# Kernel optimization log

Measured on AMD Instinct MI355X. Metric: run time of the kernel, lower is better.

The kernel has to match this reference:

```python
import jax, jax.numpy as jnp
import numpy as np

B, T, C = 2, 2048, 768
H = 12
D = C // H
HID = 4 * C
EPS = 1e-5
LS_INIT = 1e-4


def _ln(x, g, b):
    mu = jnp.mean(x, axis=-1, keepdims=True)
    var = jnp.mean((x - mu) ** 2, axis=-1, keepdims=True)
    return (x - mu) * jax.lax.rsqrt(var + EPS) * g + b


def setup_inputs() -> dict:
    key = jax.random.key(0)
    ks = jax.random.split(key, 10)
    s = lambda fan_in: 1.0 / np.sqrt(fan_in)
    return {
        "x": jax.random.normal(ks[0], (B, T, C), dtype=jnp.float32),
        "mask_logits": jnp.zeros((B, 1, T, T), dtype=jnp.float32),
        "bias": jax.random.normal(ks[1], (B, H, T, T), dtype=jnp.float32),
        "ln1_g": jnp.ones((C,), jnp.float32),
        "ln1_b": jnp.zeros((C,), jnp.float32),
        "qkv_w": jax.random.normal(ks[2], (3 * C, C), jnp.float32) * s(C),
        "qkv_b": jnp.zeros((3 * C,), jnp.float32),
        "proj_w": jax.random.normal(ks[3], (C, C), jnp.float32) * s(C),
        "proj_b": jnp.zeros((C,), jnp.float32),
        "ls1": jnp.full((C,), LS_INIT, jnp.float32),
        "ln2_g": jnp.ones((C,), jnp.float32),
        "ln2_b": jnp.zeros((C,), jnp.float32),
        "w1": jax.random.normal(ks[4], (HID, C), jnp.float32) * s(C),
        "b1": jnp.zeros((HID,), jnp.float32),
        "w2": jax.random.normal(ks[5], (C, HID), jnp.float32) * s(HID),
        "b2": jnp.zeros((C,), jnp.float32),
        "ls2": jnp.full((C,), LS_INIT, jnp.float32),
    }


def reference(x, mask_logits, bias, ln1_g, ln1_b, qkv_w, qkv_b, proj_w, proj_b,
              ls1, ln2_g, ln2_b, w1, b1, w2, b2, ls2):
    scale = 1.0 / np.sqrt(D)
    xn = _ln(x, ln1_g, ln1_b)
    qkv = xn @ qkv_w.T + qkv_b                      # [B,T,3C]
    qkv = qkv.reshape(B, T, 3, H, D).transpose(2, 0, 3, 1, 4)  # [3,B,H,T,D]
    q, k, v = qkv[0], qkv[1], qkv[2]
    logits = jnp.einsum('bhqd,bhkd->bhqk', q, k) * scale + bias + mask_logits
    attn = jax.nn.softmax(logits, axis=-1)          # [B,H,T,T]
    y = jnp.einsum('bhqk,bhkd->bhqd', attn, v)      # [B,H,T,D]
    y = y.transpose(0, 2, 1, 3).reshape(B, T, C)
    y = y @ proj_w.T + proj_b
    x = x + y * ls1
    h = _ln(x, ln2_g, ln2_b)
    h = jax.nn.gelu(h @ w1.T + b1, approximate=False)
    h = h @ w2.T + b2
    x = x + h * ls2
    return x, jax.lax.stop_gradient(attn)
```

## Files before the change

### kernel.cpp

```cpp
#include <hip/hip_runtime.h>
#include <hip/hip_bf16.h>
#include <math.h>

#define B_ 2
#define T_ 2048
#define C_ 768
#define H_ 12
#define D_ 64
#define HID_ 3072
#define NROW 4096
#define N3C 2304

typedef short bf16x8 __attribute__((ext_vector_type(8)));
typedef float f32x4 __attribute__((ext_vector_type(4)));
typedef unsigned short u16;
typedef unsigned int u32;

__device__ inline u16 f2bf(float f) {
    u32 u = __float_as_uint(f);
    u32 r = (u + 0x7fffu + ((u >> 16) & 1u)) >> 16;
    return (u16)r;
}

__global__ __launch_bounds__(256) void cvt_bf16_kernel(const float* __restrict__ s,
                                                       u16* __restrict__ d, int n) {
    int i = (blockIdx.x * 256 + threadIdx.x) * 4;
    if (i >= n) return;
    float4 v = *(const float4*)(s + i);
    ushort4 o;
    o.x = f2bf(v.x); o.y = f2bf(v.y); o.z = f2bf(v.z); o.w = f2bf(v.w);
    *(ushort4*)(d + i) = o;
}

__global__ __launch_bounds__(256) void ln_kernel(const float* __restrict__ x,
                                                 const float* __restrict__ g,
                                                 const float* __restrict__ b,
                                                 u16* __restrict__ out) {
    int row = blockIdx.x, t = threadIdx.x;
    const float* xr = x + (size_t)row * C_;
    float v[3], s = 0.f, sq = 0.f;
#pragma unroll
    for (int i = 0; i < 3; i++) {
        v[i] = xr[i * 256 + t];
        s += v[i]; sq += v[i] * v[i];
    }
    for (int m = 32; m; m >>= 1) { s += __shfl_xor(s, m); sq += __shfl_xor(sq, m); }
    __shared__ float ss[4], ssq[4];
    int wid = t >> 6;
    if ((t & 63) == 0) { ss[wid] = s; ssq[wid] = sq; }
    __syncthreads();
    s = ss[0] + ss[1] + ss[2] + ss[3];
    sq = ssq[0] + ssq[1] + ssq[2] + ssq[3];
    float mu = s * (1.f / C_);
    float var = sq * (1.f / C_) - mu * mu;
    float rstd = rsqrtf(var + 1e-5f);
#pragma unroll
    for (int i = 0; i < 3; i++) {
        int c = i * 256 + t;
        out[(size_t)row * C_ + c] = f2bf((v[i] - mu) * rstd * g[c] + b[c]);
    }
}

template <int EPI>
__global__ __launch_bounds__(256) void gemm_kernel(const u16* __restrict__ A,
                                                   const u16* __restrict__ W,
                                                   const float* __restrict__ bias,
                                                   float* __restrict__ outf,
                                                   u16* __restrict__ outb,
                                                   const float* __restrict__ res,
                                                   const float* __restrict__ ls,
                                                   int N, int K) {
    __shared__ u16 Alds[128 * 64];
    __shared__ u16 Blds[128 * 64];
    int tid = threadIdx.x;
    int m0 = blockIdx.y * 128, n0 = blockIdx.x * 128;
    int lane = tid & 63, wid = tid >> 6;
    int wr = wid >> 1, wc = wid & 1;
    int lr = lane & 15, lq = lane >> 4;

    f32x4 acc[4][4];
#pragma unroll
    for (int i = 0; i < 4; i++)
#pragma unroll
        for (int j = 0; j < 4; j++) acc[i][j] = (f32x4){0.f, 0.f, 0.f, 0.f};

    int nk = K >> 6;
    const u16* Ab = A + (size_t)m0 * K;
    const u16* Wb = W + (size_t)n0 * K;
    bf16x8 ra[4], rb[4];
#pragma unroll
    for (int i = 0; i < 4; i++) {
        int c = tid + i * 256, row = c >> 3, j = c & 7;
        ra[i] = *(const bf16x8*)(Ab + (size_t)row * K + j * 8);
        rb[i] = *(const bf16x8*)(Wb + (size_t)row * K + j * 8);
    }
    for (int kt = 0; kt < nk; ++kt) {
        __syncthreads();
#pragma unroll
        for (int i = 0; i < 4; i++) {
            int c = tid + i * 256, row = c >> 3, j = c & 7;
            int off = row * 64 + ((j ^ (row & 7)) << 3);
            *(bf16x8*)(Alds + off) = ra[i];
            *(bf16x8*)(Blds + off) = rb[i];
        }
        __syncthreads();
        if (kt + 1 < nk) {
            int k0 = (kt + 1) << 6;
#pragma unroll
            for (int i = 0; i < 4; i++) {
                int c = tid + i * 256, row = c >> 3, j = c & 7;
                ra[i] = *(const bf16x8*)(Ab + (size_t)row * K + k0 + j * 8);
                rb[i] = *(const bf16x8*)(Wb + (size_t)row * K + k0 + j * 8);
            }
        }
#pragma unroll
        for (int s = 0; s < 2; s++) {
            bf16x8 af[4], bw[4];
#pragma unroll
            for (int i = 0; i < 4; i++) {
                int arow = wr * 64 + i * 16 + lr;
                af[i] = *(const bf16x8*)(Alds + arow * 64 + (((4 * s + lq) ^ (arow & 7)) << 3));
                int brow = wc * 64 + i * 16 + lr;
                bw[i] = *(const bf16x8*)(Blds + brow * 64 + (((4 * s + lq) ^ (brow & 7)) << 3));
            }
#pragma unroll
            for (int i = 0; i < 4; i++)
#pragma unroll
                for (int j = 0; j < 4; j++)
                    acc[i][j] = __builtin_amdgcn_mfma_f32_16x16x32_bf16(af[i], bw[j], acc[i][j], 0, 0, 0);
        }
    }
#pragma unroll
    for (int i = 0; i < 4; i++) {
#pragma unroll
        for (int j = 0; j < 4; j++) {
#pragma unroll
            for (int r = 0; r < 4; r++) {
                int gm = m0 + wr * 64 + i * 16 + lq * 4 + r;
                int gn = n0 + wc * 64 + j * 16 + lr;
                float val = acc[i][j][r] + bias[gn];
                if (EPI == 0) {
                    outb[(size_t)gm * N + gn] = f2bf(val);
                } else if (EPI == 1) {
                    float gl = 0.5f * val * (1.f + erff(val * 0.70710678118654752f));
                    outb[(size_t)gm * N + gn] = f2bf(gl);
                } else {
                    outf[(size_t)gm * N + gn] = res[(size_t)gm * N + gn] + ls[gn] * val;
                }
            }
        }
    }
}

__global__ __launch_bounds__(256) void vtrans_kernel(const u16* __restrict__ qkv,
                                                     u16* __restrict__ vt) {
    __shared__ u16 tile[64 * 72];
    int t0 = blockIdx.x * 64, h = blockIdx.y, b = blockIdx.z;
    int tid = threadIdx.x;
#pragma unroll
    for (int i = 0; i < 2; i++) {
        int c = tid + i * 256, tr = c >> 3, j = c & 7;
        bf16x8 v = *(const bf16x8*)(qkv + (size_t)(b * T_ + t0 + tr) * N3C + 1536 + h * 64 + j * 8);
        *(bf16x8*)(tile + tr * 72 + j * 8) = v;
    }
    __syncthreads();
#pragma unroll
    for (int i = 0; i < 2; i++) {
        int c = tid + i * 256, d = c >> 3, tj = c & 7;
        bf16x8 o;
#pragma unroll
        for (int k = 0; k < 8; k++) o[k] = (short)tile[(tj * 8 + k) * 72 + d];
        *(bf16x8*)(vt + (size_t)((b * H_ + h) * 64 + d) * T_ + t0 + tj * 8) = o;
    }
}

__global__ __launch_bounds__(256, 2) void attn_kernel(const u16* __restrict__ qkv,
                                                      const u16* __restrict__ vt,
                                                      const float* __restrict__ bias,
                                                      const float* __restrict__ mask,
                                                      float* __restrict__ attn_out,
                                                      u16* __restrict__ ybuf) {
    __shared__ u16 S[16 * 2048];
    __shared__ float rinv_lds[16];
    char* Sb = (char*)S;
    int qt = blockIdx.x, h = blockIdx.y, b = blockIdx.z;
    int tid = threadIdx.x, lane = tid & 63, wid = tid >> 6;
    int lr = lane & 15, lq = lane >> 4;
    int q0 = qt * 16;
    size_t bh = (size_t)(b * H_ + h);
    const float scale = 0.125f;

    const u16* qp = qkv + (size_t)(b * T_ + q0 + lr) * N3C + h * 64;
    bf16x8 qa0 = *(const bf16x8*)(qp + lq * 8);
    bf16x8 qa1 = *(const bf16x8*)(qp + 32 + lq * 8);
    const float* bp = bias + (bh * T_ + q0 + lr) * T_;
    const float* mp = mask + ((size_t)b * T_ + q0 + lr) * T_;
#pragma unroll 4
    for (int ct = 0; ct < 32; ++ct) {
        int colbase = wid * 512 + ct * 16;
        const u16* kp = qkv + (size_t)(b * T_ + colbase + lr) * N3C + 768 + h * 64;
        bf16x8 kf0 = *(const bf16x8*)(kp + lq * 8);
        bf16x8 kf1 = *(const bf16x8*)(kp + 32 + lq * 8);
        float4 b4 = *(const float4*)(bp + colbase + lq * 4);
        float4 m4 = *(const float4*)(mp + colbase + lq * 4);
        f32x4 a = (f32x4){0.f, 0.f, 0.f, 0.f};
        a = __builtin_amdgcn_mfma_f32_16x16x32_bf16(kf0, qa0, a, 0, 0, 0);
        a = __builtin_amdgcn_mfma_f32_16x16x32_bf16(kf1, qa1, a, 0, 0, 0);
        ushort4 pk;
        pk.x = f2bf(a[0] * scale + b4.x + m4.x);
        pk.y = f2bf(a[1] * scale + b4.y + m4.y);
        pk.z = f2bf(a[2] * scale + b4.z + m4.z);
        pk.w = f2bf(a[3] * scale + b4.w + m4.w);
        *(ushort4*)(Sb + (((u32)lr * 4096 + 2 * colbase + 8 * lq) ^ ((lr & 7) << 4))) = pk;
    }
    __syncthreads();

    float* ao_base = attn_out + (bh * T_ + q0) * T_;
#pragma unroll 1
    for (int rr = 0; rr < 4; ++rr) {
        int r = wid * 4 + rr;
        u32 rowb = (u32)r * 4096;
        int swz = (r & 7) << 4;
        u32 pk[16];
        float mx = -1e30f;
#pragma unroll
        for (int i = 0; i < 16; i++) {
            pk[i] = *(u32*)(Sb + ((rowb + i * 256 + 4 * lane) ^ swz));
            float lo = __uint_as_float(pk[i] << 16);
            float hi = __uint_as_float(pk[i] & 0xffff0000u);
            mx = fmaxf(mx, fmaxf(lo, hi));
        }
        for (int m = 32; m; m >>= 1) mx = fmaxf(mx, __shfl_xor(mx, m));
        float e[32];
        float lsum = 0.f;
#pragma unroll
        for (int i = 0; i < 16; i++) {
            float lo = __uint_as_float(pk[i] << 16);
            float hi = __uint_as_float(pk[i] & 0xffff0000u);
            float e0 = __expf(lo - mx), e1 = __expf(hi - mx);
            e[2 * i] = e0; e[2 * i + 1] = e1;
            lsum += e0 + e1;
            u32 po = ((u32)f2bf(e1) << 16) | (u32)f2bf(e0);
            *(u32*)(Sb + ((rowb + i * 256 + 4 * lane) ^ swz)) = po;
        }
        for (int m = 32; m; m >>= 1) lsum += __shfl_xor(lsum, m);
        float rinv = 1.f / lsum;
        if (lane == 0) rinv_lds[r] = rinv;
        float* ao = ao_base + (size_t)r * T_;
#pragma unroll
        for (int i = 0; i < 16; i++) {
            float2 o;
            o.x = e[2 * i] * rinv;
            o.y = e[2 * i + 1] * rinv;
            *(float2*)(ao + i * 128 + 2 * lane) = o;
        }
    }
    __syncthreads();

    f32x4 acc = (f32x4){0.f, 0.f, 0.f, 0.f};
    const u16* vtp = vt + (bh * 64 + wid * 16 + lr) * (size_t)T_;
#pragma unroll 4
    for (int ks = 0; ks < 64; ++ks) {
        bf16x8 pf = *(const bf16x8*)(Sb + (((u32)lr * 4096 + ks * 64 + lq * 16) ^ ((lr & 7) << 4)));
        bf16x8 vf = *(const bf16x8*)(vtp + ks * 32 + lq * 8);
        acc = __builtin_amdgcn_mfma_f32_16x16x32_bf16(pf, vf, acc, 0, 0, 0);
    }
#pragma unroll
    for (int r = 0; r < 4; r++) {
        int row = lq * 4 + r;
        float y = acc[r] * rinv_lds[row];
        ybuf[(size_t)(b * T_ + q0 + row) * C_ + h * 64 + wid * 16 + lr] = f2bf(y);
    }
}

extern "C" void kernel_launch(void* const* d_in, const int* in_sizes, int n_in,
                              void* d_out, int out_size, void* d_ws, size_t ws_size,
                              hipStream_t stream) {
    const float* x = (const float*)d_in[0];
    const float* mask = (const float*)d_in[1];
    const float* bias = (const float*)d_in[2];
    const float* ln1g = (const float*)d_in[3];
    const float* ln1b = (const float*)d_in[4];
    const float* qkvw = (const float*)d_in[5];
    const float* qkvb = (const float*)d_in[6];
    const float* projw = (const float*)d_in[7];
    const float* projb = (const float*)d_in[8];
    const float* ls1 = (const float*)d_in[9];
    const float* ln2g = (const float*)d_in[10];
    const float* ln2b = (const float*)d_in[11];
    const float* w1 = (const float*)d_in[12];
    const float* b1 = (const float*)d_in[13];
    const float* w2 = (const float*)d_in[14];
    const float* b2 = (const float*)d_in[15];
    const float* ls2 = (const float*)d_in[16];

    char* ws = (char*)d_ws;
    size_t off = 0;
    u16* qkvw_b = (u16*)(ws + off); off += (size_t)N3C * C_ * 2;
    u16* projw_b = (u16*)(ws + off); off += (size_t)C_ * C_ * 2;
    u16* w1_b = (u16*)(ws + off); off += (size_t)HID_ * C_ * 2;
    u16* w2_b = (u16*)(ws + off); off += (size_t)C_ * HID_ * 2;
    u16* xn = (u16*)(ws + off); off += (size_t)NROW * C_ * 2;
    u16* qkvbuf = (u16*)(ws + off); off += (size_t)NROW * N3C * 2;
    u16* vt = (u16*)(ws + off); off += (size_t)B_ * H_ * D_ * T_ * 2;
    u16* g = qkvbuf;
    u16* ybuf = (u16*)(ws + off); off += (size_t)NROW * C_ * 2;
    float* x1 = (float*)(ws + off); off += (size_t)NROW * C_ * 4;
    (void)ws_size; (void)n_in; (void)in_sizes; (void)out_size;

    float* outx = (float*)d_out;
    float* attn_out = outx + (size_t)NROW * C_;

    cvt_bf16_kernel<<<(N3C * C_ / 4 + 255) / 256, 256, 0, stream>>>(qkvw, qkvw_b, N3C * C_);
    cvt_bf16_kernel<<<(C_ * C_ / 4 + 255) / 256, 256, 0, stream>>>(projw, projw_b, C_ * C_);
    cvt_bf16_kernel<<<(HID_ * C_ / 4 + 255) / 256, 256, 0, stream>>>(w1, w1_b, HID_ * C_);
    cvt_bf16_kernel<<<(C_ * HID_ / 4 + 255) / 256, 256, 0, stream>>>(w2, w2_b, C_ * HID_);

    ln_kernel<<<NROW, 256, 0, stream>>>(x, ln1g, ln1b, xn);
    gemm_kernel<0><<<dim3(N3C / 128, NROW / 128), 256, 0, stream>>>(
        xn, qkvw_b, qkvb, nullptr, qkvbuf, nullptr, nullptr, N3C, C_);
    vtrans_kernel<<<dim3(T_ / 64, H_, B_), 256, 0, stream>>>(qkvbuf, vt);
    attn_kernel<<<dim3(T_ / 16, H_, B_), 256, 0, stream>>>(qkvbuf, vt, bias, mask, attn_out, ybuf);
    gemm_kernel<2><<<dim3(C_ / 128, NROW / 128), 256, 0, stream>>>(
        ybuf, projw_b, projb, x1, nullptr, x, ls1, C_, C_);
    ln_kernel<<<NROW, 256, 0, stream>>>(x1, ln2g, ln2b, xn);
    gemm_kernel<1><<<dim3(HID_ / 128, NROW / 128), 256, 0, stream>>>(
        xn, w1_b, b1, nullptr, g, nullptr, nullptr, HID_, C_);
    gemm_kernel<2><<<dim3(C_ / 128, NROW / 128), 256, 0, stream>>>(
        g, w2_b, b2, outx, nullptr, x1, ls2, C_, HID_);
}
```

Before: 519.9 us.

## Split fused attention into QK-exp and PV kernels via global P buffer

Replaces the single LDS-heavy attention kernel with two kernels when the workspace is large enough. qk_kernel computes exp(logits) directly, without subtracting the row max, writes unnormalised bf16 probabilities to a global buffer and reduces the row sums. pv_kernel reads them back to write the normalised attention output and to compute P·V. The aim is to drop the 64KB LDS tile and its barriers so more blocks fit per CU. The cost is a large extra global round trip for P, and skipping the max subtraction risks overflow when logits are large.

```diff
diff --git a/kernel.cpp b/kernel.cpp
--- a/kernel.cpp
+++ b/kernel.cpp
@@ -174,6 +174,101 @@
     }
 }
 
+__global__ __launch_bounds__(256, 4) void qk_kernel(const u16* __restrict__ qkv,
+                                                    const float* __restrict__ bias,
+                                                    const float* __restrict__ mask,
+                                                    u16* __restrict__ p,
+                                                    float* __restrict__ lsum) {
+    __shared__ float red[4][16];
+    int qt = blockIdx.x, h = blockIdx.y, b = blockIdx.z;
+    int tid = threadIdx.x, lane = tid & 63, wid = tid >> 6;
+    int lr = lane & 15, lq = lane >> 4;
+    int q0 = qt * 16;
+    size_t bh = (size_t)(b * H_ + h);
+    const float scale = 0.125f;
+
+    const u16* qp = qkv + (size_t)(b * T_ + q0 + lr) * N3C + h * 64;
+    bf16x8 qa0 = *(const bf16x8*)(qp + lq * 8);
+    bf16x8 qa1 = *(const bf16x8*)(qp + 32 + lq * 8);
+    const float* bp = bias + (bh * T_ + q0 + lr) * T_ + wid * 512 + lq * 4;
+    const float* mp = mask + ((size_t)b * T_ + q0 + lr) * T_ + wid * 512 + lq * 4;
+    const u16* kbase = qkv + (size_t)(b * T_ + wid * 512 + lr) * N3C + 768 + h * 64 + lq * 8;
+    u16* pt = p + ((bh * 128 + qt) << 15) + (size_t)lr * 2048 + wid * 512 + lq * 4;
+
+    float ls = 0.f;
+#pragma unroll
+    for (int ct = 0; ct < 32; ++ct) {
+        bf16x8 kf0 = *(const bf16x8*)(kbase + (size_t)ct * 16 * N3C);
+        bf16x8 kf1 = *(const bf16x8*)(kbase + (size_t)ct * 16 * N3C + 32);
+        float4 b4 = *(const float4*)(bp + ct * 16);
+        float4 m4 = *(const float4*)(mp + ct * 16);
+        f32x4 a = (f32x4){0.f, 0.f, 0.f, 0.f};
+        a = __builtin_amdgcn_mfma_f32_16x16x32_bf16(kf0, qa0, a, 0, 0, 0);
+        a = __builtin_amdgcn_mfma_f32_16x16x32_bf16(kf1, qa1, a, 0, 0, 0);
+        float e0 = __expf(a[0] * scale + b4.x + m4.x);
+        float e1 = __expf(a[1] * scale + b4.y + m4.y);
+        float e2 = __expf(a[2] * scale + b4.z + m4.z);
+        float e3 = __expf(a[3] * scale + b4.w + m4.w);
+        ls += (e0 + e1) + (e2 + e3);
+        ushort4 pk;
+        pk.x = f2bf(e0); pk.y = f2bf(e1); pk.z = f2bf(e2); pk.w = f2bf(e3);
+        *(ushort4*)(pt + ct * 16) = pk;
+    }
+    ls += __shfl_xor(ls, 16);
+    ls += __shfl_xor(ls, 32);
+    if (lane < 16) red[wid][lr] = ls;
+    __syncthreads();
+    if (tid < 16)
+        lsum[bh * T_ + q0 + tid] = (red[0][tid] + red[1][tid]) + (red[2][tid] + red[3][tid]);
+}
+
+__global__ __launch_bounds__(256, 4) void pv_kernel(const u16* __restrict__ p,
+                                                    const u16* __restrict__ vt,
+                                                    const float* __restrict__ lsum,
+                                                    float* __restrict__ attn_out,
+                                                    u16* __restrict__ ybuf) {
+    int qt = blockIdx.x, h = blockIdx.y, b = blockIdx.z;
+    int tid = threadIdx.x, lane = tid & 63, wid = tid >> 6;
+    int lr = lane & 15, lq = lane >> 4;
+    int q0 = qt * 16;
+    size_t bh = (size_t)(b * H_ + h);
+    const u16* pt = p + ((bh * 128 + qt) << 15);
+    const float* lsb = lsum + bh * T_ + q0;
+
+    float* ao_base = attn_out + (bh * T_ + q0) * T_;
+#pragma unroll
+    for (int rr = 0; rr < 4; ++rr) {
+        int r = wid * 4 + rr;
+        float rinv = 1.f / lsb[r];
+        const u16* pr = pt + (size_t)r * 2048;
+        float* ao = ao_base + (size_t)r * T_;
+#pragma unroll
+        for (int i = 0; i < 16; i++) {
+            u32 pk2 = *(const u32*)(pr + i * 128 + 2 * lane);
+            float2 o;
+            o.x = __uint_as_float(pk2 << 16) * rinv;
+            o.y = __uint_as_float(pk2 & 0xffff0000u) * rinv;
+            *(float2*)(ao + i * 128 + 2 * lane) = o;
+        }
+    }
+
+    f32x4 acc = (f32x4){0.f, 0.f, 0.f, 0.f};
+    const u16* vtp = vt + (bh * 64 + wid * 16 + lr) * (size_t)T_ + lq * 8;
+    const u16* pr = pt + (size_t)lr * 2048 + lq * 8;
+#pragma unroll 8
+    for (int ks = 0; ks < 64; ++ks) {
+        bf16x8 pf = *(const bf16x8*)(pr + ks * 32);
+        bf16x8 vf = *(const bf16x8*)(vtp + ks * 32);
+        acc = __builtin_amdgcn_mfma_f32_16x16x32_bf16(pf, vf, acc, 0, 0, 0);
+    }
+#pragma unroll
+    for (int r = 0; r < 4; r++) {
+        int row = lq * 4 + r;
+        float y = acc[r] / lsb[row];
+        ybuf[(size_t)(b * T_ + q0 + row) * C_ + h * 64 + wid * 16 + lr] = f2bf(y);
+    }
+}
+
 __global__ __launch_bounds__(256, 2) void attn_kernel(const u16* __restrict__ qkv,
                                                       const u16* __restrict__ vt,
                                                       const float* __restrict__ bias,
@@ -193,19 +288,19 @@
     const u16* qp = qkv + (size_t)(b * T_ + q0 + lr) * N3C + h * 64;
     bf16x8 qa0 = *(const bf16x8*)(qp + lq * 8);
     bf16x8 qa1 = *(const bf16x8*)(qp + 32 + lq * 8);
-    const float* bp = bias + (bh * T_ + q0 + lr) * T_;
-    const float* mp = mask + ((size_t)b * T_ + q0 + lr) * T_;
+    const float* bp = bias + (bh * T_ + q0 + lr) * T_ + wid * 512 + lq * 4;
+    const float* mp = mask + ((size_t)b * T_ + q0 + lr) * T_ + wid * 512 + lq * 4;
+    const u16* kbase = qkv + (size_t)(b * T_ + wid * 512 + lr) * N3C + 768 + h * 64 + lq * 8;
 #pragma unroll 4
     for (int ct = 0; ct < 32; ++ct) {
-        int colbase = wid * 512 + ct * 16;
-        const u16* kp = qkv + (size_t)(b * T_ + colbase + lr) * N3C + 768 + h * 64;
-        bf16x8 kf0 = *(const bf16x8*)(kp + lq * 8);
-        bf16x8 kf1 = *(const bf16x8*)(kp + 32 + lq * 8);
-        float4 b4 = *(const float4*)(bp + colbase + lq * 4);
-        float4 m4 = *(const float4*)(mp + colbase + lq * 4);
+        bf16x8 kf0 = *(const bf16x8*)(kbase + (size_t)ct * 16 * N3C);
+        bf16x8 kf1 = *(const bf16x8*)(kbase + (size_t)ct * 16 * N3C + 32);
+        float4 b4 = *(const float4*)(bp + ct * 16);
+        float4 m4 = *(const float4*)(mp + ct * 16);
         f32x4 a = (f32x4){0.f, 0.f, 0.f, 0.f};
         a = __builtin_amdgcn_mfma_f32_16x16x32_bf16(kf0, qa0, a, 0, 0, 0);
         a = __builtin_amdgcn_mfma_f32_16x16x32_bf16(kf1, qa1, a, 0, 0, 0);
+        int colbase = wid * 512 + ct * 16;
         ushort4 pk;
         pk.x = f2bf(a[0] * scale + b4.x + m4.x);
         pk.y = f2bf(a[1] * scale + b4.y + m4.y);
@@ -232,19 +327,19 @@
         }
         for (int m = 32; m; m >>= 1) mx = fmaxf(mx, __shfl_xor(mx, m));
         float e[32];
-        float lsum = 0.f;
+        float lsumv = 0.f;
 #pragma unroll
         for (int i = 0; i < 16; i++) {
             float lo = __uint_as_float(pk[i] << 16);
             float hi = __uint_as_float(pk[i] & 0xffff0000u);
             float e0 = __expf(lo - mx), e1 = __expf(hi - mx);
             e[2 * i] = e0; e[2 * i + 1] = e1;
-            lsum += e0 + e1;
+            lsumv += e0 + e1;
             u32 po = ((u32)f2bf(e1) << 16) | (u32)f2bf(e0);
             *(u32*)(Sb + ((rowb + i * 256 + 4 * lane) ^ swz)) = po;
         }
-        for (int m = 32; m; m >>= 1) lsum += __shfl_xor(lsum, m);
-        float rinv = 1.f / lsum;
+        for (int m = 32; m; m >>= 1) lsumv += __shfl_xor(lsumv, m);
+        float rinv = 1.f / lsumv;
         if (lane == 0) rinv_lds[r] = rinv;
         float* ao = ao_base + (size_t)r * T_;
 #pragma unroll
@@ -258,11 +353,11 @@
     __syncthreads();
 
     f32x4 acc = (f32x4){0.f, 0.f, 0.f, 0.f};
-    const u16* vtp = vt + (bh * 64 + wid * 16 + lr) * (size_t)T_;
+    const u16* vtp = vt + (bh * 64 + wid * 16 + lr) * (size_t)T_ + lq * 8;
 #pragma unroll 4
     for (int ks = 0; ks < 64; ++ks) {
+        bf16x8 vf = *(const bf16x8*)(vtp + ks * 32);
         bf16x8 pf = *(const bf16x8*)(Sb + (((u32)lr * 4096 + ks * 64 + lq * 16) ^ ((lr & 7) << 4)));
-        bf16x8 vf = *(const bf16x8*)(vtp + ks * 32 + lq * 8);
         acc = __builtin_amdgcn_mfma_f32_16x16x32_bf16(pf, vf, acc, 0, 0, 0);
     }
 #pragma unroll
@@ -306,7 +401,10 @@
     u16* g = qkvbuf;
     u16* ybuf = (u16*)(ws + off); off += (size_t)NROW * C_ * 2;
     float* x1 = (float*)(ws + off); off += (size_t)NROW * C_ * 4;
-    (void)ws_size; (void)n_in; (void)in_sizes; (void)out_size;
+    u16* pbuf = (u16*)(ws + off); size_t off_p = off + (size_t)B_ * H_ * T_ * T_ * 2;
+    float* lsum = (float*)(ws + off_p); size_t off_end = off_p + (size_t)B_ * H_ * T_ * 4;
+    bool use_split = (ws_size >= off_end);
+    (void)n_in; (void)in_sizes; (void)out_size;
 
     float* outx = (float*)d_out;
     float* attn_out = outx + (size_t)NROW * C_;
@@ -320,7 +418,12 @@
     gemm_kernel<0><<<dim3(N3C / 128, NROW / 128), 256, 0, stream>>>(
         xn, qkvw_b, qkvb, nullptr, qkvbuf, nullptr, nullptr, N3C, C_);
     vtrans_kernel<<<dim3(T_ / 64, H_, B_), 256, 0, stream>>>(qkvbuf, vt);
-    attn_kernel<<<dim3(T_ / 16, H_, B_), 256, 0, stream>>>(qkvbuf, vt, bias, mask, attn_out, ybuf);
+    if (use_split) {
+        qk_kernel<<<dim3(T_ / 16, H_, B_), 256, 0, stream>>>(qkvbuf, bias, mask, pbuf, lsum);
+        pv_kernel<<<dim3(T_ / 16, H_, B_), 256, 0, stream>>>(pbuf, vt, lsum, attn_out, ybuf);
+    } else {
+        attn_kernel<<<dim3(T_ / 16, H_, B_), 256, 0, stream>>>(qkvbuf, vt, bias, mask, attn_out, ybuf);
+    }
     gemm_kernel<2><<<dim3(C_ / 128, NROW / 128), 256, 0, stream>>>(
         ybuf, projw_b, projb, x1, nullptr, x, ls1, C_, C_);
     ln_kernel<<<NROW, 256, 0, stream>>>(x1, ln2g, ln2b, xn);
```

Measured after the change: 685.7 us. 31.9% more time.
